# Performance work log

Measured on AMD Instinct MI355X. Metric: run time of the kernel, lower is better.

The kernel has to match this reference:

```python
import jax, jax.numpy as jnp
import numpy as np

D = 256      # d_model
H = 8        # nhead
HD = D // H  # head_dim
B = 16       # ragged batch size
L = 4096     # tokens per sample (equal lengths here; code handles general ragged)
NQ = 100     # instance queries per sample


def _xavier(key, shape):
    a = float(np.sqrt(6.0 / (shape[0] + shape[1])))
    return jax.random.uniform(key, shape, jnp.float32, -a, a)


def setup_inputs() -> dict:
    key = jax.random.key(0)
    ks = jax.random.split(key, 8)
    total = B * L
    source = jax.random.normal(ks[0], (total, D), jnp.float32)
    query = jax.random.normal(ks[1], (B, NQ, D), jnp.float32)
    batch_offsets = (jnp.arange(B + 1) * L).astype(jnp.int32)
    # nn.MultiheadAttention params: in-proj (split into q/k/v) + out-proj.
    Wq = _xavier(ks[2], (D, D)); bq = jnp.zeros((D,), jnp.float32)
    Wk = _xavier(ks[3], (D, D)); bk = jnp.zeros((D,), jnp.float32)
    Wv = _xavier(ks[4], (D, D)); bv = jnp.zeros((D,), jnp.float32)
    Wo = _xavier(ks[5], (D, D)); bo = jnp.zeros((D,), jnp.float32)
    return {"source": source, "query": query, "batch_offsets": batch_offsets,
            "Wq": Wq, "bq": bq, "Wk": Wk, "bk": bk, "Wv": Wv, "bv": bv,
            "Wo": Wo, "bo": bo}


def reference(source, query, batch_offsets, Wq, bq, Wk, bk, Wv, bv, Wo, bo):
    # Ragged -> padded gather (indices are concrete, computed with numpy).
    offs = np.asarray(batch_offsets)
    lens = offs[1:] - offs[:-1]                      # (B,)
    Lmax = int(lens.max())
    pos = np.arange(Lmax)
    mask = pos[None, :] < lens[:, None]              # (B, Lmax) valid keys
    idx = np.where(mask, offs[:-1, None] + pos[None, :], 0)
    kv_in = source[jnp.asarray(idx)]                 # (B, Lmax, D)

    # Projections (torch Linear: x @ W.T + b), split into heads.
    q = (query @ Wq.T + bq).reshape(B, NQ, H, HD)
    k = (kv_in @ Wk.T + bk).reshape(B, Lmax, H, HD)
    v = (kv_in @ Wv.T + bv).reshape(B, Lmax, H, HD)

    scale = 1.0 / jnp.sqrt(jnp.asarray(HD, q.dtype))
    scores = jnp.einsum("bqhd,bkhd->bhqk", q * scale, k)
    scores = jnp.where(jnp.asarray(mask)[:, None, None, :], scores, -1e30)
    attn = jax.nn.softmax(scores, axis=-1)           # (B, H, NQ, Lmax)
    ctx = jnp.einsum("bhqk,bkhd->bqhd", attn, v).reshape(B, NQ, D)
    out = ctx @ Wo.T + bo
    # Original code: dropout/norm results are discarded; residual add of query.
    return out + query
```

## Files before the change

### kernel.cpp

```cpp
#include <hip/hip_runtime.h>
#include <hip/hip_bf16.h>
#include <math.h>

#define DM     256
#define NHEAD  8
#define HDIM   32
#define QPAD   112
#define NCHUNK 8
#define BM     64
#define BN     256
#define BK     32
#define ALD    264
#define QR     4
#define CQ     4

typedef __attribute__((ext_vector_type(8))) short bf16x8;
typedef __attribute__((ext_vector_type(4))) short bf16x4;
typedef __attribute__((ext_vector_type(4))) float f32x4;

__device__ __forceinline__ short f2bf(float f) {
  union { float f; unsigned u; } x; x.f = f;
  unsigned u = (x.u + 0x7fffu + ((x.u >> 16) & 1u)) >> 16;
  return (short)u;
}
__device__ __forceinline__ float bf2f(short s) {
  union { unsigned u; float f; } x; x.u = ((unsigned)(unsigned short)s) << 16;
  return x.f;
}
__device__ __forceinline__ bf16x8 bzero8() {
  bf16x8 v;
#pragma unroll
  for (int j = 0; j < 8; j++) v[j] = (short)0;
  return v;
}
__device__ __forceinline__ bf16x8 cvt8(const float* p) {
  float4 x0 = *(const float4*)p, x1 = *(const float4*)(p + 4);
  bf16x8 v;
  v[0] = f2bf(x0.x); v[1] = f2bf(x0.y); v[2] = f2bf(x0.z); v[3] = f2bf(x0.w);
  v[4] = f2bf(x1.x); v[5] = f2bf(x1.y); v[6] = f2bf(x1.z); v[7] = f2bf(x1.w);
  return v;
}

__global__ __launch_bounds__(256) void wconv_kernel(
    const float* __restrict__ Wk, const float* __restrict__ Wv,
    short* __restrict__ Wkv) {
  int idx = blockIdx.x * 256 + threadIdx.x;
  int e0 = idx * 8;
  const float* p = (e0 < DM * DM) ? (Wk + e0) : (Wv + (e0 - DM * DM));
  *(bf16x8*)(Wkv + e0) = cvt8(p);
}

__global__ __launch_bounds__(256) void kvq_kernel(
    const float* __restrict__ src, const float* __restrict__ query,
    const float* __restrict__ Wq, const float* __restrict__ bq,
    const short* __restrict__ Wkv, const float* __restrict__ bk,
    const float* __restrict__ bv, const int* __restrict__ offs,
    short* __restrict__ Qw, short* __restrict__ Kw, short* __restrict__ Vw,
    int T, int Bn, int NQ, int Mtiles, int kvb) {
  __shared__ __align__(16) short As[BM * ALD];
  __shared__ __align__(16) float ql[QR * DM];
  int tid = threadIdx.x;

  if (blockIdx.x >= (unsigned)kvb) {
    int qbid = blockIdx.x - kvb;
    int b  = qbid / (QPAD / QR);
    int r0 = (qbid % (QPAD / QR)) * QR;
    for (int i = tid; i < QR * DM; i += 256) {
      int r = r0 + (i >> 8);
      ql[i] = (r < NQ) ? query[((size_t)b * NQ + r) * DM + (i & 255)] : 0.f;
    }
    __syncthreads();
    int d = tid;
    float bias = bq[d];
    float acc[QR];
#pragma unroll
    for (int qi = 0; qi < QR; qi++) acc[qi] = bias;
    const float* wrow = Wq + (size_t)d * DM;
    for (int k = 0; k < DM; k += 4) {
      float4 w = *(const float4*)(wrow + k);
#pragma unroll
      for (int qi = 0; qi < QR; qi++) {
        float4 x = *(const float4*)&ql[qi * DM + k];
        acc[qi] += x.x * w.x + x.y * w.y + x.z * w.z + x.w * w.w;
      }
    }
    const float scale = 0.17677669529663687f;
    int h = d >> 5, hd = d & 31;
#pragma unroll
    for (int qi = 0; qi < QR; qi++) {
      int r = r0 + qi;
      float v = (r < NQ) ? acc[qi] * scale : 0.f;
      Qw[(((size_t)b * NHEAD + h) * QPAD + r) * HDIM + hd] = f2bf(v);
    }
    return;
  }

  int bid = blockIdx.x;
  int mtile = (bid >> 4) * 8 + (bid & 7);
  int ntile = (bid >> 3) & 1;
  if (mtile >= Mtiles) return;
  int t0 = mtile * BM;
  int n0 = ntile * BN;
  bool isK = (ntile == 0);
  const float* bias = isK ? bk : bv;

  int wave = tid >> 6, lane = tid & 63;
  int l15 = lane & 15, quad = lane >> 4;

  f32x4 acc[4][4];
#pragma unroll
  for (int i = 0; i < 4; i++)
#pragma unroll
    for (int j = 0; j < 4; j++) acc[i][j] = (f32x4){0.f, 0.f, 0.f, 0.f};

  {
    int arow = tid >> 2, ac4 = tid & 3;
    int atok = t0 + arow;
    if (atok >= T) atok = T - 1;
    const float* arp = src + (size_t)atok * DM;
#pragma unroll
    for (int r = 0; r < 4; r++) {
      int c0 = r * 64 + ac4 * 16;
      const float* p = arp + c0;
      bf16x8 v0 = cvt8(p);
      bf16x8 v1 = cvt8(p + 8);
      *(bf16x8*)&As[arow * ALD + c0]     = v0;
      *(bf16x8*)&As[arow * ALD + c0 + 8] = v1;
    }
  }
  __syncthreads();

  const short* bptr = Wkv + (size_t)(n0 + wave * 64 + l15) * DM + quad * 8;
#pragma unroll
  for (int kk = 0; kk < DM; kk += BK) {
    bf16x8 bf_[4];
#pragma unroll
    for (int nt = 0; nt < 4; nt++)
      bf_[nt] = *(const bf16x8*)(bptr + (size_t)nt * 16 * DM + kk);
    bf16x8 af[4];
#pragma unroll
    for (int mt = 0; mt < 4; mt++)
      af[mt] = *(const bf16x8*)&As[(mt * 16 + l15) * ALD + kk + quad * 8];
    if (isK) {
#pragma unroll
      for (int mt = 0; mt < 4; mt++)
#pragma unroll
        for (int nt = 0; nt < 4; nt++)
          acc[mt][nt] = __builtin_amdgcn_mfma_f32_16x16x32_bf16(
              bf_[nt], af[mt], acc[mt][nt], 0, 0, 0);
    } else {
#pragma unroll
      for (int mt = 0; mt < 4; mt++)
#pragma unroll
        for (int nt = 0; nt < 4; nt++)
          acc[mt][nt] = __builtin_amdgcn_mfma_f32_16x16x32_bf16(
              af[mt], bf_[nt], acc[mt][nt], 0, 0, 0);
    }
  }

  if (isK) {
    float bk4[4][4];
    int hK[4], hdK[4];
#pragma unroll
    for (int nt = 0; nt < 4; nt++) {
      int nbq = wave * 64 + nt * 16 + quad * 4;
      float4 b4 = *(const float4*)(bias + nbq);
      bk4[nt][0] = b4.x; bk4[nt][1] = b4.y; bk4[nt][2] = b4.z; bk4[nt][3] = b4.w;
      hK[nt] = nbq >> 5;
      hdK[nt] = nbq & 31;
    }
    int bcur = 0;
#pragma unroll
    for (int mt = 0; mt < 4; mt++) {
      int tok = t0 + mt * 16 + l15;
      if (tok >= T) continue;
      while (bcur + 1 < Bn && offs[bcur + 1] <= tok) bcur++;
      int off = offs[bcur], len = offs[bcur + 1] - off;
      int l = tok - off;
      size_t bb = (size_t)off * DM;
#pragma unroll
      for (int nt = 0; nt < 4; nt++) {
        bf16x4 p;
#pragma unroll
        for (int r = 0; r < 4; r++) p[r] = f2bf(acc[mt][nt][r] + bk4[nt][r]);
        *(bf16x4*)&Kw[bb + (size_t)hK[nt] * len * HDIM + (size_t)l * HDIM +
                      hdK[nt]] = p;
      }
    }
  } else {
    float bV[4];
    int hV[4], hdV[4];
#pragma unroll
    for (int nt = 0; nt < 4; nt++) {
      int nb = wave * 64 + nt * 16 + l15;
      bV[nt] = bias[nb];
      hV[nt] = nb >> 5;
      hdV[nt] = nb & 31;
    }
    int bcur = 0;
#pragma unroll
    for (int mt = 0; mt < 4; mt++) {
      int tb = t0 + mt * 16 + quad * 4;
      if (tb >= T) continue;
      while (bcur + 1 < Bn && offs[bcur + 1] <= tb) bcur++;
      int off = offs[bcur], len = offs[bcur + 1] - off;
      size_t bb = (size_t)off * DM;
      bool span = (tb + 3 < offs[bcur + 1]) && (tb + 3 < T);
      if (span) {
        int l = tb - off;
#pragma unroll
        for (int nt = 0; nt < 4; nt++) {
          size_t idx =
              bb + (size_t)hV[nt] * len * HDIM + (size_t)hdV[nt] * len + l;
          bf16x4 p;
#pragma unroll
          for (int r = 0; r < 4; r++) p[r] = f2bf(acc[mt][nt][r] + bV[nt]);
          if ((idx & 3) == 0) {
            *(bf16x4*)&Vw[idx] = p;
          } else {
#pragma unroll
            for (int r = 0; r < 4; r++) Vw[idx + r] = p[r];
          }
        }
      } else {
        int bc2 = bcur;
#pragma unroll
        for (int r = 0; r < 4; r++) {
          int tok = tb + r;
          if (tok >= T) continue;
          while (bc2 + 1 < Bn && offs[bc2 + 1] <= tok) bc2++;
          int off2 = offs[bc2], len2 = offs[bc2 + 1] - off2;
          int l = tok - off2;
          size_t bb2 = (size_t)off2 * DM;
#pragma unroll
          for (int nt = 0; nt < 4; nt++)
            Vw[bb2 + (size_t)hV[nt] * len2 * HDIM + (size_t)hdV[nt] * len2 +
               l] = f2bf(acc[mt][nt][r] + bV[nt]);
        }
      }
    }
  }
}

__global__ __launch_bounds__(448) void attn_kernel(
    const short* __restrict__ Qw, const short* __restrict__ Kw,
    const short* __restrict__ Vw, const int* __restrict__ offs,
    short* __restrict__ Ops, float* __restrict__ Ml, int Bn) {
  int c  = blockIdx.x % NCHUNK;
  int bh = blockIdx.x / NCHUNK;
  int h = bh % NHEAD, b = bh / NHEAD;
  int wave = threadIdx.x >> 6, lane = threadIdx.x & 63;
  int l15 = lane & 15, quad = lane >> 4;

  int off = offs[b], len = offs[b + 1] - off;
  int cl = ((len + NCHUNK * 32 - 1) / (NCHUNK * 32)) * 32;
  int kstart = c * cl;
  int kend   = min(kstart + cl, len);

  const short* Kh = Kw + (size_t)off * DM + (size_t)h * len * HDIM;
  const short* Vh = Vw + (size_t)off * DM + (size_t)h * len * HDIM;

  int row16 = wave * 16 + l15;
  bf16x8 aq = *(const bf16x8*)(
      Qw + (((size_t)b * NHEAD + h) * QPAD + row16) * HDIM + quad * 8);

  f32x4 o[2];
#pragma unroll
  for (int j = 0; j < 2; j++) o[j] = (f32x4){0.f, 0.f, 0.f, 0.f};
  float mrun[4], lrun[4];
#pragma unroll
  for (int r = 0; r < 4; r++) { mrun[r] = -1e30f; lrun[r] = 0.f; }

  __shared__ __align__(16) short plds[7][16][72];

  for (int kb = kstart; kb < kend; kb += 64) {
    bool valid[4];
    bf16x8 bk_[4];
#pragma unroll
    for (int nt = 0; nt < 4; nt++) {
      int key = kb + nt * 16 + l15;
      valid[nt] = key < kend;
      bk_[nt] = valid[nt]
                    ? *(const bf16x8*)(Kh + (size_t)key * HDIM + quad * 8)
                    : bzero8();
    }
    f32x4 zero = {0.f, 0.f, 0.f, 0.f};
    f32x4 s[4];
#pragma unroll
    for (int nt = 0; nt < 4; nt++)
      s[nt] = __builtin_amdgcn_mfma_f32_16x16x32_bf16(aq, bk_[nt], zero, 0, 0, 0);
#pragma unroll
    for (int r = 0; r < 4; r++) {
      float v0 = valid[0] ? s[0][r] : -1e30f;
      float v1 = valid[1] ? s[1][r] : -1e30f;
      float v2 = valid[2] ? s[2][r] : -1e30f;
      float v3 = valid[3] ? s[3][r] : -1e30f;
      float t = fmaxf(fmaxf(v0, v1), fmaxf(v2, v3));
      t = fmaxf(t, __shfl_xor(t, 1, 16));
      t = fmaxf(t, __shfl_xor(t, 2, 16));
      t = fmaxf(t, __shfl_xor(t, 4, 16));
      t = fmaxf(t, __shfl_xor(t, 8, 16));
      float mn = fmaxf(mrun[r], t);
      float al = __expf(mrun[r] - mn);
      float p0 = valid[0] ? __expf(v0 - mn) : 0.f;
      float p1 = valid[1] ? __expf(v1 - mn) : 0.f;
      float p2 = valid[2] ? __expf(v2 - mn) : 0.f;
      float p3 = valid[3] ? __expf(v3 - mn) : 0.f;
      float rs = (p0 + p1) + (p2 + p3);
      rs += __shfl_xor(rs, 1, 16);
      rs += __shfl_xor(rs, 2, 16);
      rs += __shfl_xor(rs, 4, 16);
      rs += __shfl_xor(rs, 8, 16);
      lrun[r] = al * lrun[r] + rs;
      mrun[r] = mn;
      o[0][r] *= al;
      o[1][r] *= al;
      plds[wave][quad * 4 + r][l15]      = f2bf(p0);
      plds[wave][quad * 4 + r][16 + l15] = f2bf(p1);
      plds[wave][quad * 4 + r][32 + l15] = f2bf(p2);
      plds[wave][quad * 4 + r][48 + l15] = f2bf(p3);
    }
    bf16x8 pa0 = *(const bf16x8*)&plds[wave][l15][quad * 8];
    bf16x8 pa1 = *(const bf16x8*)&plds[wave][l15][32 + quad * 8];
    bf16x8 bv_[2][2];
#pragma unroll
    for (int half = 0; half < 2; half++) {
#pragma unroll
      for (int ht = 0; ht < 2; ht++) {
        int hd = ht * 16 + l15;
        int k0 = kb + half * 32 + quad * 8;
        const short* p = Vh + (size_t)hd * len + k0;
        if (k0 + 7 < len) {
          bv_[half][ht] = *(const bf16x8*)p;
        } else {
          bf16x8 v;
#pragma unroll
          for (int j = 0; j < 8; j++) v[j] = (k0 + j < len) ? p[j] : (short)0;
          bv_[half][ht] = v;
        }
      }
    }
#pragma unroll
    for (int ht = 0; ht < 2; ht++) {
      o[ht] = __builtin_amdgcn_mfma_f32_16x16x32_bf16(pa0, bv_[0][ht], o[ht],
                                                      0, 0, 0);
      o[ht] = __builtin_amdgcn_mfma_f32_16x16x32_bf16(pa1, bv_[1][ht], o[ht],
                                                      0, 0, 0);
    }
  }

#pragma unroll
  for (int r = 0; r < 4; r++) {
    int row = wave * 16 + quad * 4 + r;
    size_t base = (((size_t)c * Bn + b) * NHEAD + h) * QPAD + row;
#pragma unroll
    for (int ht = 0; ht < 2; ht++)
      Ops[base * HDIM + ht * 16 + l15] = f2bf(o[ht][r]);
    if (l15 == 0) {
      Ml[base * 2]     = mrun[r];
      Ml[base * 2 + 1] = lrun[r];
    }
  }
}

__global__ __launch_bounds__(256) void combine_kernel(
    const short* __restrict__ Ops, const float* __restrict__ Ml,
    const float* __restrict__ query, const float* __restrict__ Wo,
    const float* __restrict__ bo, float* __restrict__ out, int Bn, int NQ) {
  int bpb = (NQ + CQ - 1) / CQ;
  int b  = blockIdx.x / bpb;
  int q0 = (blockIdx.x % bpb) * CQ;
  int tid = threadIdx.x;

  __shared__ __align__(16) short opsl[CQ][NCHUNK][DM];
  __shared__ float mll[NCHUNK][NHEAD][CQ][2];
  __shared__ __align__(16) float ctx[CQ * DM];

  for (int t = tid; t < CQ * NCHUNK * (DM / 8); t += 256) {
    int q   = t / (NCHUNK * 32);
    int rem = t % (NCHUNK * 32);
    int c   = rem / 32;
    int v   = rem % 32;
    int h   = v >> 2;
    int hd0 = (v & 3) * 8;
    int qq = q0 + q;
    if (qq >= NQ) qq = NQ - 1;
    size_t base = (((size_t)c * Bn + b) * NHEAD + h) * QPAD + qq;
    *(bf16x8*)&opsl[q][c][v * 8] = *(const bf16x8*)&Ops[base * HDIM + hd0];
  }
  for (int t = tid; t < CQ * NCHUNK * NHEAD; t += 256) {
    int q   = t / (NCHUNK * NHEAD);
    int rem = t % (NCHUNK * NHEAD);
    int c   = rem / NHEAD;
    int h   = rem % NHEAD;
    int qq = q0 + q;
    if (qq >= NQ) qq = NQ - 1;
    size_t base = (((size_t)c * Bn + b) * NHEAD + h) * QPAD + qq;
    mll[c][h][q][0] = Ml[base * 2];
    mll[c][h][q][1] = Ml[base * 2 + 1];
  }
  __syncthreads();

  int d = tid, h = d >> 5;
#pragma unroll
  for (int qi = 0; qi < CQ; qi++) {
    float M = -1e30f;
#pragma unroll
    for (int c = 0; c < NCHUNK; c++) M = fmaxf(M, mll[c][h][qi][0]);
    float L = 0.f, acc = 0.f;
#pragma unroll
    for (int c = 0; c < NCHUNK; c++) {
      float w = __expf(mll[c][h][qi][0] - M);
      L += mll[c][h][qi][1] * w;
      acc += w * bf2f(opsl[qi][c][d]);
    }
    ctx[qi * DM + d] = (L > 0.f) ? acc / L : 0.f;
  }
  __syncthreads();

  const float* wrow = Wo + (size_t)d * DM;
  float acc[CQ];
  float bias = bo[d];
#pragma unroll
  for (int qi = 0; qi < CQ; qi++) acc[qi] = bias;
  for (int k = 0; k < DM; k += 4) {
    float4 w = *(const float4*)(wrow + k);
#pragma unroll
    for (int qi = 0; qi < CQ; qi++) {
      float4 x = *(const float4*)&ctx[qi * DM + k];
      acc[qi] += x.x * w.x + x.y * w.y + x.z * w.z + x.w * w.w;
    }
  }
#pragma unroll
  for (int qi = 0; qi < CQ; qi++) {
    int q = q0 + qi;
    if (q < NQ)
      out[((size_t)b * NQ + q) * DM + d] =
          acc[qi] + query[((size_t)b * NQ + q) * DM + d];
  }
}

extern "C" void kernel_launch(void* const* d_in, const int* in_sizes, int n_in,
                              void* d_out, int out_size, void* d_ws,
                              size_t ws_size, hipStream_t stream) {
  const float* src   = (const float*)d_in[0];
  const float* query = (const float*)d_in[1];
  const int*   offs  = (const int*)d_in[2];
  const float* Wq = (const float*)d_in[3];
  const float* bq = (const float*)d_in[4];
  const float* Wk = (const float*)d_in[5];
  const float* bk = (const float*)d_in[6];
  const float* Wv = (const float*)d_in[7];
  const float* bv = (const float*)d_in[8];
  const float* Wo = (const float*)d_in[9];
  const float* bo = (const float*)d_in[10];
  float* out = (float*)d_out;

  int T  = in_sizes[0] / DM;
  int Bn = in_sizes[2] - 1;
  int NQ = in_sizes[1] / (Bn * DM);

  char* w = (char*)d_ws;
  size_t qsz = (size_t)Bn * NHEAD * QPAD * HDIM * 2;
  size_t ksz = (size_t)T * DM * 2;
  size_t osz = (size_t)NCHUNK * Bn * NHEAD * QPAD * HDIM * 2;
  size_t msz = (size_t)NCHUNK * Bn * NHEAD * QPAD * 2 * 4;
  short* Qw  = (short*)w;
  short* Kw  = (short*)(w + qsz);
  short* Vw  = (short*)(w + qsz + ksz);
  short* Ops = (short*)(w + qsz + 2 * ksz);
  float* Mlp = (float*)(w + qsz + 2 * ksz + osz);
  short* Wkv = (short*)(w + qsz + 2 * ksz + osz + msz);

  int Mtiles = (T + BM - 1) / BM;
  int groups = (Mtiles + 7) / 8;
  int kvb = groups * 16;
  int nqb = Bn * (QPAD / QR);

  wconv_kernel<<<(2 * DM * DM) / (256 * 8), 256, 0, stream>>>(Wk, Wv, Wkv);
  kvq_kernel<<<kvb + nqb, 256, 0, stream>>>(
      src, query, Wq, bq, Wkv, bk, bv, offs, Qw, Kw, Vw, T, Bn, NQ, Mtiles,
      kvb);
  attn_kernel<<<Bn * NHEAD * NCHUNK, 448, 0, stream>>>(Qw, Kw, Vw, offs, Ops,
                                                       Mlp, Bn);
  combine_kernel<<<Bn * ((NQ + CQ - 1) / CQ), 256, 0, stream>>>(
      Ops, Mlp, query, Wo, bo, out, Bn, NQ);
}
```

Before: 248.7 us.

## Compute Q projection with bf16 MFMA tiles inside the K/V GEMM kernel

Replaces the scalar fp32 Q-projection blocks with MFMA GEMM tiles that reuse the K/V projection path. Wq is converted to bf16 with the softmax scale folded in, and the padded Q workspace is zeroed with a memset instead of explicit zero writes. The combine kernel's query-rows-per-block constant is also lowered from 4 to 2. The Q projection now rounds its inputs to bf16 before the matmul, and the change adds a memset launch.

```diff
diff --git a/kernel.cpp b/kernel.cpp
--- a/kernel.cpp
+++ b/kernel.cpp
@@ -11,8 +11,7 @@
 #define BN     256
 #define BK     32
 #define ALD    264
-#define QR     4
-#define CQ     4
+#define CQ     2
 
 typedef __attribute__((ext_vector_type(8))) short bf16x8;
 typedef __attribute__((ext_vector_type(4))) short bf16x4;
@@ -40,72 +39,71 @@
   v[4] = f2bf(x1.x); v[5] = f2bf(x1.y); v[6] = f2bf(x1.z); v[7] = f2bf(x1.w);
   return v;
 }
+__device__ __forceinline__ bf16x8 cvt8s(const float* p, float s) {
+  float4 x0 = *(const float4*)p, x1 = *(const float4*)(p + 4);
+  bf16x8 v;
+  v[0] = f2bf(x0.x * s); v[1] = f2bf(x0.y * s);
+  v[2] = f2bf(x0.z * s); v[3] = f2bf(x0.w * s);
+  v[4] = f2bf(x1.x * s); v[5] = f2bf(x1.y * s);
+  v[6] = f2bf(x1.z * s); v[7] = f2bf(x1.w * s);
+  return v;
+}
 
 __global__ __launch_bounds__(256) void wconv_kernel(
     const float* __restrict__ Wk, const float* __restrict__ Wv,
-    short* __restrict__ Wkv) {
+    const float* __restrict__ Wq, short* __restrict__ Wkvq) {
   int idx = blockIdx.x * 256 + threadIdx.x;
   int e0 = idx * 8;
-  const float* p = (e0 < DM * DM) ? (Wk + e0) : (Wv + (e0 - DM * DM));
-  *(bf16x8*)(Wkv + e0) = cvt8(p);
-}
-
-__global__ __launch_bounds__(256) void kvq_kernel(
+  const float* p;
+  float s = 1.f;
+  if (e0 < DM * DM) {
+    p = Wk + e0;
+  } else if (e0 < 2 * DM * DM) {
+    p = Wv + (e0 - DM * DM);
+  } else {
+    p = Wq + (e0 - 2 * DM * DM);
+    s = 0.17677669529663687f;
+  }
+  *(bf16x8*)(Wkvq + e0) = cvt8s(p, s);
+}
+
+__global__ __launch_bounds__(256) void kv_gemm_kernel(
     const float* __restrict__ src, const float* __restrict__ query,
-    const float* __restrict__ Wq, const float* __restrict__ bq,
-    const short* __restrict__ Wkv, const float* __restrict__ bk,
-    const float* __restrict__ bv, const int* __restrict__ offs,
-    short* __restrict__ Qw, short* __restrict__ Kw, short* __restrict__ Vw,
-    int T, int Bn, int NQ, int Mtiles, int kvb) {
-  __shared__ __align__(16) short As[BM * ALD];
-  __shared__ __align__(16) float ql[QR * DM];
+    const short* __restrict__ Wkvq, const float* __restrict__ bq,
+    const float* __restrict__ bk, const float* __restrict__ bv,
+    const int* __restrict__ offs, short* __restrict__ Qw,
+    short* __restrict__ Kw, short* __restrict__ Vw, int T, int Bn, int NQ,
+    int Mtiles, int kvb) {
+  int bid = blockIdx.x;
   int tid = threadIdx.x;
-
-  if (blockIdx.x >= (unsigned)kvb) {
-    int qbid = blockIdx.x - kvb;
-    int b  = qbid / (QPAD / QR);
-    int r0 = (qbid % (QPAD / QR)) * QR;
-    for (int i = tid; i < QR * DM; i += 256) {
-      int r = r0 + (i >> 8);
-      ql[i] = (r < NQ) ? query[((size_t)b * NQ + r) * DM + (i & 255)] : 0.f;
-    }
-    __syncthreads();
-    int d = tid;
-    float bias = bq[d];
-    float acc[QR];
-#pragma unroll
-    for (int qi = 0; qi < QR; qi++) acc[qi] = bias;
-    const float* wrow = Wq + (size_t)d * DM;
-    for (int k = 0; k < DM; k += 4) {
-      float4 w = *(const float4*)(wrow + k);
-#pragma unroll
-      for (int qi = 0; qi < QR; qi++) {
-        float4 x = *(const float4*)&ql[qi * DM + k];
-        acc[qi] += x.x * w.x + x.y * w.y + x.z * w.z + x.w * w.w;
-      }
-    }
-    const float scale = 0.17677669529663687f;
-    int h = d >> 5, hd = d & 31;
-#pragma unroll
-    for (int qi = 0; qi < QR; qi++) {
-      int r = r0 + qi;
-      float v = (r < NQ) ? acc[qi] * scale : 0.f;
-      Qw[(((size_t)b * NHEAD + h) * QPAD + r) * HDIM + hd] = f2bf(v);
-    }
-    return;
-  }
-
-  int bid = blockIdx.x;
-  int mtile = (bid >> 4) * 8 + (bid & 7);
-  int ntile = (bid >> 3) & 1;
-  if (mtile >= Mtiles) return;
-  int t0 = mtile * BM;
-  int n0 = ntile * BN;
-  bool isK = (ntile == 0);
-  const float* bias = isK ? bk : bv;
-
   int wave = tid >> 6, lane = tid & 63;
   int l15 = lane & 15, quad = lane >> 4;
+
+  bool isQ = (bid >= kvb);
+  const float* Asrc;
+  int Arows, t0, n0;
+  bool swapped;
+  bool isK = false;
+  if (isQ) {
+    int qt = bid - kvb;
+    t0 = qt * BM;
+    Asrc = query;
+    Arows = Bn * NQ;
+    n0 = 2 * DM;
+    swapped = true;
+  } else {
+    int mtile = (bid >> 4) * 8 + (bid & 7);
+    int ntile = (bid >> 3) & 1;
+    if (mtile >= Mtiles) return;
+    t0 = mtile * BM;
+    n0 = ntile * BN;
+    isK = (ntile == 0);
+    swapped = isK;
+    Asrc = src;
+    Arows = T;
+  }
+
+  __shared__ __align__(16) short As[BM * ALD];
 
   f32x4 acc[4][4];
 #pragma unroll
@@ -116,8 +114,8 @@
   {
     int arow = tid >> 2, ac4 = tid & 3;
     int atok = t0 + arow;
-    if (atok >= T) atok = T - 1;
-    const float* arp = src + (size_t)atok * DM;
+    if (atok >= Arows) atok = Arows - 1;
+    const float* arp = Asrc + (size_t)atok * DM;
 #pragma unroll
     for (int r = 0; r < 4; r++) {
       int c0 = r * 64 + ac4 * 16;
@@ -130,7 +128,7 @@
   }
   __syncthreads();
 
-  const short* bptr = Wkv + (size_t)(n0 + wave * 64 + l15) * DM + quad * 8;
+  const short* bptr = Wkvq + (size_t)(n0 + wave * 64 + l15) * DM + quad * 8;
 #pragma unroll
   for (int kk = 0; kk < DM; kk += BK) {
     bf16x8 bf_[4];
@@ -141,7 +139,7 @@
 #pragma unroll
     for (int mt = 0; mt < 4; mt++)
       af[mt] = *(const bf16x8*)&As[(mt * 16 + l15) * ALD + kk + quad * 8];
-    if (isK) {
+    if (swapped) {
 #pragma unroll
       for (int mt = 0; mt < 4; mt++)
 #pragma unroll
@@ -158,7 +156,36 @@
     }
   }
 
-  if (isK) {
+  if (isQ) {
+    const float scale = 0.17677669529663687f;
+    float bq4[4][4];
+    int hQ[4], hdQ[4];
+#pragma unroll
+    for (int nt = 0; nt < 4; nt++) {
+      int nbq = wave * 64 + nt * 16 + quad * 4;
+      float4 b4 = *(const float4*)(bq + nbq);
+      bq4[nt][0] = b4.x * scale; bq4[nt][1] = b4.y * scale;
+      bq4[nt][2] = b4.z * scale; bq4[nt][3] = b4.w * scale;
+      hQ[nt] = nbq >> 5;
+      hdQ[nt] = nbq & 31;
+    }
+#pragma unroll
+    for (int mt = 0; mt < 4; mt++) {
+      int row = t0 + mt * 16 + l15;
+      if (row >= Arows) continue;
+      int b = row / NQ;
+      int q = row - b * NQ;
+#pragma unroll
+      for (int nt = 0; nt < 4; nt++) {
+        bf16x4 p;
+#pragma unroll
+        for (int r = 0; r < 4; r++) p[r] = f2bf(acc[mt][nt][r] + bq4[nt][r]);
+        *(bf16x4*)&Qw[(((size_t)b * NHEAD + hQ[nt]) * QPAD + q) * HDIM +
+                      hdQ[nt]] = p;
+      }
+    }
+  } else if (isK) {
+    const float* bias = bk;
     float bk4[4][4];
     int hK[4], hdK[4];
 #pragma unroll
@@ -188,6 +215,7 @@
       }
     }
   } else {
+    const float* bias = bv;
     float bV[4];
     int hV[4], hdV[4];
 #pragma unroll
@@ -470,17 +498,18 @@
   short* Vw  = (short*)(w + qsz + ksz);
   short* Ops = (short*)(w + qsz + 2 * ksz);
   float* Mlp = (float*)(w + qsz + 2 * ksz + osz);
-  short* Wkv = (short*)(w + qsz + 2 * ksz + osz + msz);
+  short* Wkvq = (short*)(w + qsz + 2 * ksz + osz + msz);
 
   int Mtiles = (T + BM - 1) / BM;
   int groups = (Mtiles + 7) / 8;
   int kvb = groups * 16;
-  int nqb = Bn * (QPAD / QR);
-
-  wconv_kernel<<<(2 * DM * DM) / (256 * 8), 256, 0, stream>>>(Wk, Wv, Wkv);
-  kvq_kernel<<<kvb + nqb, 256, 0, stream>>>(
-      src, query, Wq, bq, Wkv, bk, bv, offs, Qw, Kw, Vw, T, Bn, NQ, Mtiles,
-      kvb);
+  int qtiles = (Bn * NQ + BM - 1) / BM;
+
+  hipMemsetAsync(Qw, 0, qsz, stream);
+  wconv_kernel<<<(3 * DM * DM) / (256 * 8), 256, 0, stream>>>(Wk, Wv, Wq,
+                                                              Wkvq);
+  kv_gemm_kernel<<<kvb + qtiles, 256, 0, stream>>>(
+      src, query, Wkvq, bq, bk, bv, offs, Qw, Kw, Vw, T, Bn, NQ, Mtiles, kvb);
   attn_kernel<<<Bn * NHEAD * NCHUNK, 448, 0, stream>>>(Qw, Kw, Vw, offs, Ops,
                                                        Mlp, Bn);
   combine_kernel<<<Bn * ((NQ + CQ - 1) / CQ), 256, 0, stream>>>(
```

After: 250.3 us. About the same (+0.6%).
